# Kernel optimization log

Measured on AMD Instinct MI355X. Metric: run time of the kernel, lower is better.

## Reference

```python
import jax, jax.numpy as jnp
import numpy as np

DIM = 768
FS = 48          # feature_size; H = W = FS, N = FS*FS
HEADS = 8


def _linear_params(key, fin, fout):
    k1, k2 = jax.random.split(key)
    s = 1.0 / np.sqrt(fin)
    W = jax.random.uniform(k1, (fin, fout), minval=-s, maxval=s, dtype=jnp.float32)
    b = jax.random.uniform(k2, (fout,), minval=-s, maxval=s, dtype=jnp.float32)
    return W, b


def setup_inputs() -> dict:
    key = jax.random.key(0)
    ks = jax.random.split(key, 12)
    B, C, H, W = 1, DIM, FS, FS
    N = H * W
    x = jax.random.normal(ks[0], (B, C, H, W), dtype=jnp.float32)
    y = jax.random.normal(ks[1], (B, C, H, W), dtype=jnp.float32)
    Wqx, bqx = _linear_params(ks[2], C, 3 * C)
    Wqy, bqy = _linear_params(ks[3], C, 3 * C)
    Wqxc, bqxc = _linear_params(ks[4], N, 3 * N)
    Wqyc, bqyc = _linear_params(ks[5], N, 3 * N)
    Wpxc, bpxc = _linear_params(ks[6], N, N)
    Wpyc, bpyc = _linear_params(ks[7], N, N)
    Wax, bax = _linear_params(ks[8], C, C)
    Way, bay = _linear_params(ks[9], C, C)
    return {"x": x, "y": y,
            "Wqx": Wqx, "bqx": bqx, "Wqy": Wqy, "bqy": bqy,
            "Wqxc": Wqxc, "bqxc": bqxc, "Wqyc": Wqyc, "bqyc": bqyc,
            "Wpxc": Wpxc, "bpxc": bpxc, "Wpyc": Wpyc, "bpyc": bpyc,
            "Wax": Wax, "bax": bax, "Way": Way, "bay": bay}


def reference(x, y, Wqx, bqx, Wqy, bqy, Wqxc, bqxc, Wqyc, bqyc,
              Wpxc, bpxc, Wpyc, bpyc, Wax, bax, Way, bay):
    B, C, H, W = x.shape
    N = H * W
    h = HEADS
    hd = C // h            # spatial head dim
    hdc = N // h           # channel head dim
    scale = hd ** (-0.5)
    scale_c = hdc ** (-0.5)

    def spatial_qkv(t, Wq, bq):
        t_ = t.transpose(0, 2, 3, 1).reshape(B, N, C)          # [B,N,C]
        qkv = (t_ @ Wq + bq).reshape(B, N, 3, h, hd)
        qkv = qkv.transpose(2, 0, 3, 1, 4).reshape(3, B * h, N, hd)
        return qkv[0], qkv[1], qkv[2]

    def channel_qkv(t, Wq, bq):
        tc = t.reshape(B, C, N)                                 # [B,C,N]
        qkv = (tc @ Wq + bq).reshape(B, C, 3, h, hdc)
        qkv = qkv.transpose(2, 0, 3, 1, 4).reshape(3, B * h, C, hdc)
        return qkv[0], qkv[1], qkv[2]

    qx, kx, vx = spatial_qkv(x, Wqx, bqx)
    qy, ky, vy = spatial_qkv(y, Wqy, bqy)
    qxc, kxc, vxc = channel_qkv(x, Wqxc, bqxc)
    qyc, kyc, vyc = channel_qkv(y, Wqyc, bqyc)

    # spatial self-attention (x with x, y with y): scores [B*h, N, N]
    ax = jax.nn.softmax((qx * scale) @ kx.transpose(0, 2, 1), axis=-1)
    ay = jax.nn.softmax((qy * scale) @ ky.transpose(0, 2, 1), axis=-1)
    # channel cross-attention (x queries attend to y keys/values and vice versa): scores [B*h, C, C]
    axc = jax.nn.softmax((qxc * scale_c) @ kyc.transpose(0, 2, 1), axis=-1)
    ayc = jax.nn.softmax((qyc * scale_c) @ kxc.transpose(0, 2, 1), axis=-1)

    # NOTE: reshape(B, N, -1) on the [B*h, N, hd] layout (no head transpose) replicates the
    # original torch code exactly.
    x_self = ((ax @ vx).reshape(B, N, C) @ Wax + bax).reshape(B, H, W, C).transpose(0, 3, 1, 2)
    y_self = ((ay @ vy).reshape(B, N, C) @ Way + bay).reshape(B, H, W, C).transpose(0, 3, 1, 2)
    x_ch = ((axc @ vyc).reshape(B, C, N) @ Wpxc + bpxc).reshape(B, C, H, W)
    y_ch = ((ayc @ vxc).reshape(B, C, N) @ Wpyc + bpyc).reshape(B, C, H, W)

    return (x_self + x_ch, y_self + y_ch)
```

## Files before the change

### kernel.cpp

```cpp
#include <hip/hip_runtime.h>
#include <math.h>

typedef unsigned short u16;
typedef unsigned int u32;
typedef short bf16x8 __attribute__((ext_vector_type(8)));
typedef float f32x4 __attribute__((ext_vector_type(4)));
typedef float f32x16 __attribute__((ext_vector_type(16)));

__device__ __forceinline__ float bf2f(u16 u) {
  union { unsigned int i; float f; } v;
  v.i = ((unsigned int)u) << 16;
  return v.f;
}
__device__ __forceinline__ u16 f2bf(float f) {
  union { float f; unsigned int i; } v;
  v.f = f;
  unsigned int u = v.i;
  return (u16)((u + 0x7fffu + ((u >> 16) & 1u)) >> 16);
}
__device__ __forceinline__ u32 pkbf(float a, float b) {
  u32 d;
  asm("v_cvt_pk_bf16_f32 %0, %1, %2" : "=v"(d) : "v"(a), "v"(b));
  return d;
}

__device__ __forceinline__ void glds16(const u16* g, u16* l) {
  __builtin_amdgcn_global_load_lds(
      (const __attribute__((address_space(1))) void*)g,
      (__attribute__((address_space(3))) void*)l, 16, 0, 0);
}

__global__ __launch_bounds__(256) void probe_dtype(const u32* __restrict__ xw,
                                                   int nwords, int* flag)
{
  const int tid = threadIdx.x;
  int cnt = 0;
  for (int i = tid; i < nwords; i += 256) {
    u32 w = xw[i];
    u32 e = (w >> 7) & 0xFFu;
    if (e >= 110u && e <= 140u) cnt++;
  }
#pragma unroll
  for (int off = 32; off >= 1; off >>= 1) cnt += __shfl_xor(cnt, off);
  __shared__ int s[4];
  if ((tid & 63) == 0) s[tid >> 6] = cnt;
  __syncthreads();
  if (tid == 0) {
    int tot = s[0] + s[1] + s[2] + s[3];
    flag[0] = (tot < nwords / 2) ? 1 : 0;
  }
}

__global__ __launch_bounds__(256) void gemm128(
    const u16* __restrict__ A, int lda, long sAz,
    const u16* __restrict__ B, int ldb, long sBz,
    const u16* __restrict__ bias, int sBiasZ,
    void* __restrict__ OutV, int ldo, long sOz, long oOff, int outMode,
    const int* __restrict__ flagp,
    float scale, int M, int Nn, int K)
{
  const int z = blockIdx.z;
  const u16* Ab = A + (long)z * sAz;
  const u16* Bb = B + (long)z * sBz;
  const int bm = blockIdx.y * 128;
  const int bn = blockIdx.x * 128;

  __shared__ u16 As[2][128 * 32];
  __shared__ u16 Bs[2][128 * 32];

  const int tid  = threadIdx.x;
  const int lane = tid & 63;
  const int wave = tid >> 6;
  const int wr = wave >> 1, wc = wave & 1;
  const int q = lane >> 4, l15 = lane & 15;

  f32x4 acc[4][4];
#pragma unroll
  for (int i = 0; i < 4; i++)
#pragma unroll
    for (int j = 0; j < 4; j++) acc[i][j] = (f32x4){0.f, 0.f, 0.f, 0.f};

  const int srow = tid >> 2;
  const int sc8  = (tid & 3) * 8;
  const u16* aptr = Ab + (long)(bm + srow) * lda + sc8;
  const u16* bptr = Bb + (long)(bn + srow) * ldb + sc8;

  auto stage = [&](int buf, int k0) {
    u16* asl = As[buf] + tid * 8;
    u16* bsl = Bs[buf] + tid * 8;
    glds16(aptr + k0, asl);
    glds16(aptr + (long)64 * lda + k0, asl + 256 * 8);
    glds16(bptr + k0, bsl);
    glds16(bptr + (long)64 * ldb + k0, bsl + 256 * 8);
  };
  auto compute = [&](int buf) {
    bf16x8 af[4], bfr[4];
#pragma unroll
    for (int mi = 0; mi < 4; mi++)
      af[mi] = *(const bf16x8*)(As[buf] + (wr * 64 + mi * 16 + l15) * 32 + q * 8);
#pragma unroll
    for (int nj = 0; nj < 4; nj++)
      bfr[nj] = *(const bf16x8*)(Bs[buf] + (wc * 64 + nj * 16 + l15) * 32 + q * 8);
#pragma unroll
    for (int mi = 0; mi < 4; mi++)
#pragma unroll
      for (int nj = 0; nj < 4; nj++)
        acc[mi][nj] = __builtin_amdgcn_mfma_f32_16x16x32_bf16(af[mi], bfr[nj], acc[mi][nj], 0, 0, 0);
  };

  stage(0, 0);
  __syncthreads();
  int cur = 0;
  for (int k0 = 32; k0 < K; k0 += 32) {
    stage(cur ^ 1, k0);
    compute(cur);
    __syncthreads();
    cur ^= 1;
  }
  compute(cur);

  const int flagv = (outMode == 2) ? *flagp : 0;
  const bool storeF32 = (outMode == 1) || (outMode == 2 && flagv);
  const u16* bz = bias ? bias + (long)z * sBiasZ : nullptr;
#pragma unroll
  for (int mi = 0; mi < 4; mi++) {
    const int r0 = bm + wr * 64 + mi * 16 + q * 4;
#pragma unroll
    for (int nj = 0; nj < 4; nj++) {
      const int col = bn + wc * 64 + nj * 16 + l15;
      const float bsv = bz ? bf2f(bz[col]) : 0.0f;
      if (storeF32) {
        float* Out = (float*)OutV + oOff + (long)z * sOz;
#pragma unroll
        for (int r = 0; r < 4; r++)
          Out[(long)(r0 + r) * ldo + col] = acc[mi][nj][r] * scale + bsv;
      } else {
        u16* Out = (u16*)OutV + oOff + (long)z * sOz;
#pragma unroll
        for (int r = 0; r < 4; r++)
          Out[(long)(r0 + r) * ldo + col] = f2bf(acc[mi][nj][r] * scale + bsv);
      }
    }
  }
}

__global__ __launch_bounds__(256) void flashS(
    const u16* __restrict__ QKV, long sTz,
    const u16* __restrict__ VTb, long sVz,
    u16* __restrict__ Out, long sOz,
    int ldq, int Mq, float scl)
{
  const int bm = blockIdx.x * 128;
  const int h  = blockIdx.y;
  const int t  = blockIdx.z;
  const int h96 = h * 96;
  const u16* qB  = QKV + (long)t * sTz;
  const u16* kB  = qB + 768;
  const u16* vtB = VTb + (long)t * sVz + (long)h96 * Mq;
  u16* oB = Out + (long)t * sOz + (long)h * Mq * 96;

  __shared__ u16 KsL[2][64 * 128];
  __shared__ u16 VsL[2][96 * 64];

  const int tid  = threadIdx.x;
  const int lane = tid & 63;
  const int wave = tid >> 6;
  const int l31  = lane & 31;
  const int hi   = lane >> 5;

  bf16x8 qf[6];
  {
    const u16* qrow = qB + (long)(bm + wave * 32 + l31) * ldq + h96;
#pragma unroll
    for (int cs = 0; cs < 6; cs++) {
      union { bf16x8 v; u16 e[8]; } a, b;
      a.v = *(const bf16x8*)(qrow + cs * 16 + hi * 8);
#pragma unroll
      for (int e = 0; e < 8; e++) b.e[e] = f2bf(bf2f(a.e[e]) * scl);
      qf[cs] = b.v;
    }
  }

  f32x16 accO[3];
#pragma unroll
  for (int r = 0; r < 16; r++) { accO[0][r] = 0.f; accO[1][r] = 0.f; accO[2][r] = 0.f; }
  float m_r = -1e30f, l_r = 0.f;

  auto stageKV = [&](int buf, int k0) {
    const u16* kBase = kB + (long)k0 * ldq + h96;
#pragma unroll
    for (int i = 0; i < 4; i++) {
      const int G = tid + 256 * i;
      const int row = G >> 4;
      const int g = (G & 15) ^ (row & 7);
      const u16* src = (g < 12) ? (kBase + (long)row * ldq + g * 8) : kB;
      glds16(src, &KsL[buf][G * 8]);
    }
    const u16* vBase = vtB + k0;
#pragma unroll
    for (int i = 0; i < 3; i++) {
      const int G = tid + 256 * i;
      const int row = G >> 3;
      const int g = (G & 7) ^ (row & 7);
      glds16(vBase + (long)row * Mq + g * 8, &VsL[buf][G * 8]);
    }
  };
  auto ldK = [&](int buf, int kt2, int cs) -> bf16x8 {
    const int row = kt2 * 32 + l31;
    const int g = (2 * cs + hi) ^ (row & 7);
    return *(const bf16x8*)(&KsL[buf][row * 128 + g * 8]);
  };
  auto ldV = [&](int buf, int dt, int s) -> bf16x8 {
    const int row = dt * 32 + l31;
    const int g = (2 * s + hi) ^ (row & 7);
    return *(const bf16x8*)(&VsL[buf][row * 64 + g * 8]);
  };

  stageKV(0, 0);
  __syncthreads();
  int cur = 0;
  const int nt = Mq / 64;
  for (int kt = 0; kt < nt; kt++) {
    if (kt + 1 < nt) stageKV(cur ^ 1, (kt + 1) * 64);

    f32x16 sA, sB;
#pragma unroll
    for (int r = 0; r < 16; r++) { sA[r] = 0.f; sB[r] = 0.f; }
#pragma unroll
    for (int cs = 0; cs < 6; cs++) {
      sA = __builtin_amdgcn_mfma_f32_32x32x16_bf16(ldK(cur, 0, cs), qf[cs], sA, 0, 0, 0);
      sB = __builtin_amdgcn_mfma_f32_32x32x16_bf16(ldK(cur, 1, cs), qf[cs], sB, 0, 0, 0);
    }

    float tm = -1e30f;
#pragma unroll
    for (int r = 0; r < 16; r++) tm = fmaxf(tm, fmaxf(sA[r], sB[r]));
    tm = fmaxf(tm, __shfl_xor(tm, 32));
    if (!__all(tm <= m_r + 8.f)) {
      const float mn = fmaxf(m_r, tm);
      const float al = __expf(m_r - mn);
      m_r = mn; l_r *= al;
#pragma unroll
      for (int r = 0; r < 16; r++) {
        const float a = __shfl(al, (r & 3) + 8 * (r >> 2) + 4 * hi);
        accO[0][r] *= a; accO[1][r] *= a; accO[2][r] *= a;
      }
    }
    float rs = 0.f;
#pragma unroll
    for (int r = 0; r < 16; r++) {
      sA[r] = __expf(sA[r] - m_r); rs += sA[r];
      sB[r] = __expf(sB[r] - m_r); rs += sB[r];
    }
    rs += __shfl_xor(rs, 32);
    l_r += rs;

#pragma unroll
    for (int s = 0; s < 4; s++) {
      const f32x16& P = (s < 2) ? sA : sB;
      const int rb = (s & 1) * 8;
      u32 X  = pkbf(P[rb + 0], P[rb + 1]);
      u32 X2 = pkbf(P[rb + 2], P[rb + 3]);
      u32 Y  = pkbf(P[rb + 4], P[rb + 5]);
      u32 Y2 = pkbf(P[rb + 6], P[rb + 7]);
      asm volatile("v_permlane32_swap_b32 %0, %1" : "+v"(X), "+v"(Y));
      asm volatile("v_permlane32_swap_b32 %0, %1" : "+v"(X2), "+v"(Y2));
      union { u32 w[4]; bf16x8 v; } pa;
      pa.w[0] = X; pa.w[1] = X2; pa.w[2] = Y; pa.w[3] = Y2;
#pragma unroll
      for (int dt = 0; dt < 3; dt++)
        accO[dt] = __builtin_amdgcn_mfma_f32_32x32x16_bf16(pa.v, ldV(cur, dt, s), accO[dt], 0, 0, 0);
    }

    __syncthreads();
    cur ^= 1;
  }

  const float inv = 1.0f / l_r;
#pragma unroll
  for (int r = 0; r < 16; r++) {
    const int row = (r & 3) + 8 * (r >> 2) + 4 * hi;
    const float iv = __shfl(inv, row);
    const long rowb = (long)(bm + wave * 32 + row) * 96;
#pragma unroll
    for (int dt = 0; dt < 3; dt++)
      oB[rowb + dt * 32 + l31] = f2bf(accO[dt][r] * iv);
  }
}

__global__ __launch_bounds__(256) void gemm_pv(
    const u16* __restrict__ P, int ldP, long sPz,
    const u16* __restrict__ Vt, int ldVt, long sVz,
    u16* __restrict__ Out, int ldo, long sOz, int K)
{
  const int z = blockIdx.z;
  const u16* Pz = P + (long)z * sPz;
  const u16* Vz = Vt + (long)z * sVz;
  u16* Oz = Out + (long)z * sOz;
  const int bm = blockIdx.y * 64;
  const int bn = blockIdx.x * 96;

  __shared__ u16 As[2][64 * 32];
  __shared__ u16 Bs[2][96 * 32];

  const int tid  = threadIdx.x;
  const int lane = tid & 63;
  const int wave = tid >> 6;
  const int wr = wave >> 1, wc = wave & 1;
  const int q = lane >> 4, l15 = lane & 15;

  f32x4 acc[2][3];
#pragma unroll
  for (int i = 0; i < 2; i++)
#pragma unroll
    for (int j = 0; j < 3; j++) acc[i][j] = (f32x4){0.f, 0.f, 0.f, 0.f};

  const int srow = lane >> 2;
  const int sc8  = (lane & 3) * 8;

  const u16* aRow = Pz + (long)(bm + wave * 16 + srow) * ldP + sc8;
  const u16* bRow0 = nullptr; const u16* bRow1 = nullptr;
  if (wave < 3) {
    bRow0 = Vz + (long)(bn + (2 * wave) * 16 + srow) * ldVt + sc8;
    bRow1 = Vz + (long)(bn + (2 * wave + 1) * 16 + srow) * ldVt + sc8;
  }

  auto stage = [&](int buf, int k0) {
    glds16(aRow + k0, As[buf] + wave * 512 + lane * 8);
    if (wave < 3) {
      glds16(bRow0 + k0, Bs[buf] + (2 * wave) * 512 + lane * 8);
      glds16(bRow1 + k0, Bs[buf] + (2 * wave + 1) * 512 + lane * 8);
    }
  };
  auto compute = [&](int buf) {
    bf16x8 af[2], bfr[3];
#pragma unroll
    for (int mi = 0; mi < 2; mi++)
      af[mi] = *(const bf16x8*)(As[buf] + (wr * 32 + mi * 16 + l15) * 32 + q * 8);
#pragma unroll
    for (int nj = 0; nj < 3; nj++)
      bfr[nj] = *(const bf16x8*)(Bs[buf] + (wc * 48 + nj * 16 + l15) * 32 + q * 8);
#pragma unroll
    for (int mi = 0; mi < 2; mi++)
#pragma unroll
      for (int nj = 0; nj < 3; nj++)
        acc[mi][nj] = __builtin_amdgcn_mfma_f32_16x16x32_bf16(af[mi], bfr[nj], acc[mi][nj], 0, 0, 0);
  };

  stage(0, 0);
  __syncthreads();
  int cur = 0;
  for (int k0 = 32; k0 < K; k0 += 32) {
    stage(cur ^ 1, k0);
    compute(cur);
    __syncthreads();
    cur ^= 1;
  }
  compute(cur);

#pragma unroll
  for (int mi = 0; mi < 2; mi++) {
    const int r0 = bm + wr * 32 + mi * 16 + q * 4;
#pragma unroll
    for (int nj = 0; nj < 3; nj++) {
      const int cl = bn + wc * 48 + nj * 16 + l15;
#pragma unroll
      for (int r = 0; r < 4; r++)
        Oz[(long)(r0 + r) * ldo + cl] = f2bf(acc[mi][nj][r]);
    }
  }
}

#define BM 64
#define BN 64
#define BK 32
#define LDSP (BK + 8)

__global__ __launch_bounds__(256) void gemm64(
    const void* __restrict__ Av, int lda, long sAz, int aExt,
    const void* __restrict__ Bv, int ldb, long sBz, int bNT, int bExt,
    const void* __restrict__ biasv,
    void* __restrict__ OutV, int ldo, long sOz, long oOff, int outMode,
    const int* __restrict__ flagp,
    float scale, int M, int Nn, int K)
{
  const int flagv = *flagp;
  const bool aF32 = aExt && flagv;
  const bool bF32 = bExt && flagv;

  const int z = blockIdx.z;
  const int bm = blockIdx.y * BM;
  const int bn = blockIdx.x * BN;

  __shared__ u16 As[BM][LDSP];
  __shared__ u16 Bs[BN][LDSP];

  const int tid  = threadIdx.x;
  const int lane = tid & 63;
  const int wave = tid >> 6;
  const int wr = wave >> 1;
  const int wc = wave & 1;
  const int q   = lane >> 4;
  const int l15 = lane & 15;

  f32x4 acc[2][2];
#pragma unroll
  for (int i = 0; i < 2; i++)
#pragma unroll
    for (int j = 0; j < 2; j++) acc[i][j] = (f32x4){0.f, 0.f, 0.f, 0.f};

  const int am  = tid >> 2;
  const int ach = (tid & 3) * 8;

  for (int k0 = 0; k0 < K; k0 += BK) {
    __syncthreads();
    if (aF32) {
      const float* src = (const float*)Av + (long)z * sAz + (long)(bm + am) * lda + (k0 + ach);
      f32x4 f0 = *(const f32x4*)src;
      f32x4 f1 = *(const f32x4*)(src + 4);
      u16 t[8] = {f2bf(f0[0]), f2bf(f0[1]), f2bf(f0[2]), f2bf(f0[3]),
                  f2bf(f1[0]), f2bf(f1[1]), f2bf(f1[2]), f2bf(f1[3])};
      *(uint4*)(&As[am][ach]) = *(const uint4*)t;
    } else {
      const u16* src = (const u16*)Av + (long)z * sAz + (long)(bm + am) * lda + (k0 + ach);
      *(uint4*)(&As[am][ach]) = *(const uint4*)src;
    }
    if (bNT) {
      if (bF32) {
        u16 t[8] = {0, 0, 0, 0, 0, 0, 0, 0};
        if (bn + am < Nn) {
          const float* src = (const float*)Bv + (long)z * sBz + (long)(bn + am) * ldb + (k0 + ach);
          f32x4 f0 = *(const f32x4*)src;
          f32x4 f1 = *(const f32x4*)(src + 4);
#pragma unroll
          for (int j = 0; j < 4; j++) { t[j] = f2bf(f0[j]); t[4 + j] = f2bf(f1[j]); }
        }
        *(uint4*)(&Bs[am][ach]) = *(const uint4*)t;
      } else {
        uint4 val = make_uint4(0u, 0u, 0u, 0u);
        if (bn + am < Nn)
          val = *(const uint4*)((const u16*)Bv + (long)z * sBz + (long)(bn + am) * ldb + (k0 + ach));
        *(uint4*)(&Bs[am][ach]) = val;
      }
    } else {
      const int kk = tid >> 3;
      const int n0 = (tid & 7) * 8;
      if (bn + n0 < Nn) {
        if (bF32) {
          const float* src = (const float*)Bv + (long)z * sBz + (long)(k0 + kk) * ldb + (bn + n0);
          f32x4 f0 = *(const f32x4*)src;
          f32x4 f1 = *(const f32x4*)(src + 4);
#pragma unroll
          for (int j = 0; j < 4; j++) {
            Bs[n0 + j][kk] = f2bf(f0[j]);
            Bs[n0 + 4 + j][kk] = f2bf(f1[j]);
          }
        } else {
          uint4 val = *(const uint4*)((const u16*)Bv + (long)z * sBz + (long)(k0 + kk) * ldb + (bn + n0));
          const u16* pv = (const u16*)&val;
#pragma unroll
          for (int j = 0; j < 8; j++) Bs[n0 + j][kk] = pv[j];
        }
      } else {
#pragma unroll
        for (int j = 0; j < 8; j++) Bs[n0 + j][kk] = 0;
      }
    }
    __syncthreads();

    bf16x8 af[2], bfr[2];
#pragma unroll
    for (int t = 0; t < 2; t++)
      af[t] = *(const bf16x8*)(&As[wr * 32 + t * 16 + l15][q * 8]);
#pragma unroll
    for (int t = 0; t < 2; t++)
      bfr[t] = *(const bf16x8*)(&Bs[wc * 32 + t * 16 + l15][q * 8]);
#pragma unroll
    for (int i = 0; i < 2; i++)
#pragma unroll
      for (int j = 0; j < 2; j++)
        acc[i][j] = __builtin_amdgcn_mfma_f32_16x16x32_bf16(af[i], bfr[j], acc[i][j], 0, 0, 0);
  }

#pragma unroll
  for (int i = 0; i < 2; i++) {
    const int r0 = bm + wr * 32 + i * 16 + q * 4;
#pragma unroll
    for (int j = 0; j < 2; j++) {
      const int col = bn + wc * 32 + j * 16 + l15;
      if (col >= Nn) continue;
      float bsv = 0.0f;
      if (biasv) bsv = flagv ? ((const float*)biasv)[col] : bf2f(((const u16*)biasv)[col]);
      const bool storeF32 = (outMode == 1) || (outMode == 2 && flagv);
      if (storeF32) {
        float* Out = (float*)OutV + oOff + (long)z * sOz;
#pragma unroll
        for (int r = 0; r < 4; r++)
          Out[(long)(r0 + r) * ldo + col] = acc[i][j][r] * scale + bsv;
      } else {
        u16* Out = (u16*)OutV + oOff + (long)z * sOz;
#pragma unroll
        for (int r = 0; r < 4; r++)
          Out[(long)(r0 + r) * ldo + col] = f2bf(acc[i][j][r] * scale + bsv);
      }
    }
  }
}

__global__ __launch_bounds__(256) void softmax_rows(
    float* S, int ldS, long sSz,
    u16* P, int ldP, long sPz, int ncols)
{
  const int row = blockIdx.x;
  const int z = blockIdx.y;
  float* s = S + (long)z * sSz + (long)row * ldS;
  u16*   p = P + (long)z * sPz + (long)row * ldP;
  const int tid = threadIdx.x;
  const int lane = tid & 63, wave = tid >> 6;

  float v[9];
  int cnt = 0;
  float mx = -1e30f;
  for (int c = tid; c < ncols; c += 256) {
    float t = s[c];
    v[cnt++] = t;
    mx = fmaxf(mx, t);
  }
#pragma unroll
  for (int off = 32; off >= 1; off >>= 1) mx = fmaxf(mx, __shfl_xor(mx, off));
  __shared__ float redm[4];
  __shared__ float reds[4];
  if (lane == 0) redm[wave] = mx;
  __syncthreads();
  mx = fmaxf(fmaxf(redm[0], redm[1]), fmaxf(redm[2], redm[3]));

  float sum = 0.f;
  for (int i = 0; i < cnt; i++) { v[i] = __expf(v[i] - mx); sum += v[i]; }
#pragma unroll
  for (int off = 32; off >= 1; off >>= 1) sum += __shfl_xor(sum, off);
  if (lane == 0) reds[wave] = sum;
  __syncthreads();
  sum = reds[0] + reds[1] + reds[2] + reds[3];
  const float inv = 1.0f / sum;

  cnt = 0;
  for (int c = tid; c < ncols; c += 256) p[c] = f2bf(v[cnt++] * inv);
}

__global__ __launch_bounds__(256) void transpose_in(
    const void* __restrict__ tinv, u16* __restrict__ outp,
    const int* __restrict__ flagp, int inRows, int inCols)
{
  const bool f32 = *flagp != 0;
  __shared__ u16 tile[32][33];
  const int bx = blockIdx.x * 32;
  const int by = blockIdx.y * 32;
  const int tx = threadIdx.x & 31;
  const int ty = threadIdx.x >> 5;
#pragma unroll
  for (int k = 0; k < 4; k++) {
    const long idx = (long)(by + ty + k * 8) * inCols + bx + tx;
    tile[ty + k * 8][tx] = f32 ? f2bf(((const float*)tinv)[idx]) : ((const u16*)tinv)[idx];
  }
  __syncthreads();
#pragma unroll
  for (int k = 0; k < 4; k++) {
    const int j = bx + ty + k * 8;
    const int i = by + tx;
    outp[(long)j * inRows + i] = tile[tx][ty + k * 8];
  }
}

__global__ __launch_bounds__(256) void transpose_v(
    const u16* __restrict__ src, int ldsrc,
    u16* __restrict__ dst, int lddst, int rows, int cols)
{
  __shared__ u16 tile[32][33];
  const int bx = blockIdx.x * 32;
  const int by = blockIdx.y * 32;
  const int tx = threadIdx.x & 31;
  const int ty = threadIdx.x >> 5;
#pragma unroll
  for (int k = 0; k < 4; k++)
    tile[ty + k * 8][tx] = src[(long)(by + ty + k * 8) * ldsrc + bx + tx];
  __syncthreads();
#pragma unroll
  for (int k = 0; k < 4; k++)
    dst[(long)(bx + ty + k * 8) * lddst + by + tx] = tile[tx][ty + k * 8];
}

__global__ __launch_bounds__(256) void cvt_flat(
    const void* __restrict__ src, u16* __restrict__ dst,
    const int* __restrict__ flagp, long n)
{
  const bool f32 = *flagp != 0;
  long i = ((long)blockIdx.x * 256 + threadIdx.x) * 4;
  if (i + 3 < n) {
    if (f32) {
      f32x4 v = *(const f32x4*)((const float*)src + i);
#pragma unroll
      for (int j = 0; j < 4; j++) dst[i + j] = f2bf(v[j]);
    } else {
      *(uint2*)(dst + i) = *(const uint2*)((const u16*)src + i);
    }
  }
}

struct P8 { const void* p[8]; };
__global__ __launch_bounds__(256) void cvt_bias(P8 s, u16* __restrict__ dst,
                                                const int* __restrict__ flagp)
{
  const bool f32 = *flagp != 0;
  const int sizes[8] = {2304, 2304, 6912, 6912, 2304, 2304, 768, 768};
  int gid = blockIdx.x * 256 + threadIdx.x;
  int seg = 0, off = gid;
  while (seg < 8 && off >= sizes[seg]) { off -= sizes[seg]; seg++; }
  if (seg >= 8) return;
  float v = f32 ? ((const float*)s.p[seg])[off] : bf2f(((const u16*)s.p[seg])[off]);
  dst[gid] = f2bf(v);
}

__global__ __launch_bounds__(256) void transpose_add_out(
    const u16* __restrict__ tin, void* outv, long oOff,
    const int* __restrict__ flagp, int inRows, int inCols)
{
  const bool f32 = *flagp != 0;
  __shared__ u16 tile[32][33];
  const int bx = blockIdx.x * 32;
  const int by = blockIdx.y * 32;
  const int tx = threadIdx.x & 31;
  const int ty = threadIdx.x >> 5;
#pragma unroll
  for (int k = 0; k < 4; k++)
    tile[ty + k * 8][tx] = tin[(long)(by + ty + k * 8) * inCols + bx + tx];
  __syncthreads();
#pragma unroll
  for (int k = 0; k < 4; k++) {
    const int j = bx + ty + k * 8;
    const int i = by + tx;
    const long idx = (long)j * inRows + i;
    const float val = bf2f(tile[tx][ty + k * 8]);
    if (f32) {
      float* o = (float*)outv + oOff;
      o[idx] = o[idx] + val;
    } else {
      u16* o = (u16*)outv + oOff;
      o[idx] = f2bf(bf2f(o[idx]) + val);
    }
  }
}

extern "C" void kernel_launch(void* const* d_in, const int* in_sizes, int n_in,
                              void* d_out, int out_size, void* d_ws, size_t ws_size,
                              hipStream_t stream)
{
  const int N = 2304, C = 768, HD = 96, HDC = 288;
  const size_t NC = (size_t)N * C;

  const void* x    = d_in[0];
  const void* y    = d_in[1];
  const void* Wqx  = d_in[2];  const void* bqx  = d_in[3];
  const void* Wqy  = d_in[4];  const void* bqy  = d_in[5];
  const void* Wqxc = d_in[6];  const void* bqxc = d_in[7];
  const void* Wqyc = d_in[8];  const void* bqyc = d_in[9];
  const void* Wpxc = d_in[10]; const void* bpxc = d_in[11];
  const void* Wpyc = d_in[12]; const void* bpyc = d_in[13];
  const void* Wax  = d_in[14]; const void* bax  = d_in[15];
  const void* Way  = d_in[16]; const void* bay  = d_in[17];

  char* base = (char*)d_ws;
  int* flag = (int*)base;
  size_t off = 256;
  auto alloc16 = [&](size_t elems) -> u16* {
    u16* p = (u16*)(base + off);
    off = (off + elems * 2 + 255) & ~(size_t)255;
    return p;
  };

  u16* WqxT  = alloc16((size_t)2304 * 768);
  u16* WqyT  = alloc16((size_t)2304 * 768);
  u16* WqxcT = alloc16((size_t)6912 * 2304);
  u16* WqycT = alloc16((size_t)6912 * 2304);
  u16* WpxcT = alloc16((size_t)2304 * 2304);
  u16* WpycT = alloc16((size_t)2304 * 2304);
  u16* WaxT  = alloc16((size_t)768 * 768);
  u16* WayT  = alloc16((size_t)768 * 768);
  u16* biasB = alloc16(24576);
  u16* xb = alloc16(NC);
  u16* yb = alloc16(NC);
  u16* RT = alloc16(2 * NC);
  u16* RQ1 = alloc16(3 * NC);
  u16* RQ2 = alloc16(3 * NC);
  u16* RS = alloc16(2 * NC);
  u16* VT = alloc16(2 * NC);
  size_t fixedEnd = off;
  float* Sbuf = (float*)(base + fixedEnd);
  size_t availS = ws_size > fixedEnd ? ws_size - fixedEnd : 0;

  const size_t spHead = (size_t)N * N * 4;
  const bool fat = ws_size >= fixedEnd + spHead;

  auto G64 = [&](const void* A, int lda, long sAz, int aExt,
                 const void* B, int ldb, long sBz, int bNT, int bExt,
                 const void* bias, void* Out, int ldo, long sOz, long oOff, int outMode,
                 float scale, int M, int Nn, int K, int Z) {
    dim3 grid((Nn + BN - 1) / BN, (M + BM - 1) / BM, Z);
    gemm64<<<grid, 256, 0, stream>>>(A, lda, sAz, aExt, B, ldb, sBz, bNT, bExt,
                                     bias, Out, ldo, sOz, oOff, outMode, flag,
                                     scale, M, Nn, K);
  };
  auto G128 = [&](const u16* A, int lda, long sAz,
                  const u16* B, int ldb, long sBz,
                  const u16* bias, int sBiasZ,
                  void* Out, int ldo, long sOz, long oOff, int outMode,
                  float scale, int M, int Nn, int K, int Z) {
    dim3 grid(Nn / 128, M / 128, Z);
    gemm128<<<grid, 256, 0, stream>>>(A, lda, sAz, B, ldb, sBz, bias, sBiasZ,
                                      Out, ldo, sOz, oOff, outMode, flag,
                                      scale, M, Nn, K);
  };

  probe_dtype<<<1, 256, 0, stream>>>((const u32*)x, 1024, flag);

  if (fat) {
    transpose_in<<<dim3(2304 / 32, 768 / 32),  256, 0, stream>>>(Wqx,  WqxT,  flag, 768,  2304);
    transpose_in<<<dim3(2304 / 32, 768 / 32),  256, 0, stream>>>(Wqy,  WqyT,  flag, 768,  2304);
    transpose_in<<<dim3(6912 / 32, 2304 / 32), 256, 0, stream>>>(Wqxc, WqxcT, flag, 2304, 6912);
    transpose_in<<<dim3(6912 / 32, 2304 / 32), 256, 0, stream>>>(Wqyc, WqycT, flag, 2304, 6912);
    transpose_in<<<dim3(2304 / 32, 2304 / 32), 256, 0, stream>>>(Wpxc, WpxcT, flag, 2304, 2304);
    transpose_in<<<dim3(2304 / 32, 2304 / 32), 256, 0, stream>>>(Wpyc, WpycT, flag, 2304, 2304);
    transpose_in<<<dim3(768 / 32, 768 / 32),   256, 0, stream>>>(Wax,  WaxT,  flag, 768,  768);
    transpose_in<<<dim3(768 / 32, 768 / 32),   256, 0, stream>>>(Way,  WayT,  flag, 768,  768);
    P8 bp; bp.p[0] = bqx; bp.p[1] = bqy; bp.p[2] = bqxc; bp.p[3] = bqyc;
    bp.p[4] = bpxc; bp.p[5] = bpyc; bp.p[6] = bax; bp.p[7] = bay;
    cvt_bias<<<96, 256, 0, stream>>>(bp, biasB, flag);
    const u16 *bqxB = biasB, *bqxcB = biasB + 4608,
              *bpxcB = biasB + 18432, *baxB = biasB + 23040;
    cvt_flat<<<(unsigned)(NC / 4 / 256), 256, 0, stream>>>(x, xb, flag, (long)NC);
    cvt_flat<<<(unsigned)(NC / 4 / 256), 256, 0, stream>>>(y, yb, flag, (long)NC);
    u16 *xt = RT, *yt = RT + NC;
    transpose_in<<<dim3(N / 32, C / 32), 256, 0, stream>>>(x, xt, flag, C, N);
    transpose_in<<<dim3(N / 32, C / 32), 256, 0, stream>>>(y, yt, flag, C, N);

    auto attF = [&](const u16* qB, const u16* kB, const u16* vB, int ldq,
                    u16* att, int Mq, int hd, float scl) {
      transpose_v<<<dim3((8 * hd) / 32, Mq / 32), 256, 0, stream>>>(vB, ldq, VT, Mq, Mq, 8 * hd);
      const long perHead = (long)Mq * Mq * 4;
      int nb = (int)(availS / perHead);
      if (nb > 8) nb = 8;
      for (int h0 = 0; h0 < 8; h0 += nb) {
        const int zc = (8 - h0 < nb) ? 8 - h0 : nb;
        G128(qB + h0 * hd, ldq, hd, kB + h0 * hd, ldq, hd, nullptr, 0,
             Sbuf, Mq, (long)Mq * Mq, 0, 1, scl, Mq, Mq, hd, zc);
        softmax_rows<<<dim3(Mq, zc), 256, 0, stream>>>(Sbuf, Mq, (long)Mq * Mq,
            (u16*)Sbuf, 2 * Mq, (long)Mq * 2 * Mq, Mq);
        gemm_pv<<<dim3(hd / 96, Mq / 64, zc), 256, 0, stream>>>(
            (const u16*)Sbuf, 2 * Mq, (long)Mq * 2 * Mq,
            VT + (long)h0 * hd * Mq, Mq, (long)hd * Mq,
            att + (long)h0 * Mq * hd, hd, (long)Mq * hd, Mq);
      }
    };

    u16 *qkvxs = RQ1;
    G128(xt, C, (long)NC, WqxT, C, (long)NC, bqxB, 3 * C,
         qkvxs, 3 * C, 3 * (long)NC, 0, 0, 1.f, N, 3 * C, C, 2);

    u16 *qkvys = RQ2;
    u16 *attx = RT;
    const float sscale = 1.0f / sqrtf(96.0f);
    transpose_v<<<dim3((8 * HD) / 32, N / 32), 256, 0, stream>>>(
        qkvxs + 2 * C, 3 * C, VT, N, N, 8 * HD);
    transpose_v<<<dim3((8 * HD) / 32, N / 32), 256, 0, stream>>>(
        qkvys + 2 * C, 3 * C, VT + NC, N, N, 8 * HD);
    flashS<<<dim3(N / 128, 8, 2), 256, 0, stream>>>(
        qkvxs, 3 * (long)NC, VT, (long)NC, attx, (long)NC, 3 * C, N, sscale);

    u16 *xself = RS;
    G128(attx, C, (long)NC, WaxT, C, (long)768 * 768, baxB, C,
         xself, C, (long)NC, 0, 0, 1.f, N, C, C, 2);

    u16 *qkvxc = RQ1, *qkvyc = RQ2;
    G128(xb, N, (long)NC, WqxcT, N, (long)6912 * 2304, bqxcB, 3 * N,
         qkvxc, 3 * N, 3 * (long)NC, 0, 0, 1.f, C, 3 * N, N, 2);

    u16 *attxc = RT, *attyc = RT + NC;
    const float cscale = 1.0f / sqrtf(288.0f);
    attF(qkvxc, qkvyc + N, qkvyc + 2 * N, 3 * N, attxc, C, HDC, cscale);
    attF(qkvyc, qkvxc + N, qkvxc + 2 * N, 3 * N, attyc, C, HDC, cscale);

    G128(attxc, N, (long)NC, WpxcT, N, (long)2304 * 2304, bpxcB, N,
         d_out, N, (long)NC, 0, 2, 1.f, C, N, N, 2);

    transpose_add_out<<<dim3(C / 32, N / 32), 256, 0, stream>>>(xself, d_out, 0, flag, N, C);
    transpose_add_out<<<dim3(C / 32, N / 32), 256, 0, stream>>>(RS + NC, d_out, (long)NC, flag, N, C);
    return;
  }

  {
    char* b2 = (char*)d_ws;
    u16* RA = (u16*)(b2 + 256);
    u16* RB = RA + 3 * NC;
    u16* RD = RB + 3 * NC;
    u16* RE = RD + 2 * NC;
    const size_t offSsp = 256 + (size_t)(8 * NC) * 2;
    float* Ssp = (float*)(b2 + offSsp);
    const size_t availSp = ws_size > offSsp ? ws_size - offSsp : 0;
    const size_t offSch = 256 + (size_t)(10 * NC) * 2;
    float* Sch = (float*)(b2 + offSch);
    const size_t availCh = ws_size > offSch ? ws_size - offSch : 0;

    u16 *xt = RD, *yt = RD + NC;
    u16 *qkvxs = RA, *qkvys = RB;
    u16 *attx = RD, *atty = RD + NC;
    u16 *xself = RE, *yself = RE + NC;
    u16 *qkvxc = RA, *qkvyc = RB;
    u16 *attxc = RD, *attyc = RD + NC;

    auto attention = [&](const u16* qB, const u16* kB, const u16* vB, int ldq,
                         u16* att, int Mq, int hd, float scl,
                         float* S, size_t availBytes) {
      const long perHead = (long)Mq * Mq * 4;
      int nb = (int)(availBytes / perHead);
      if (nb > 8) nb = 8;
      if (nb >= 1) {
        for (int h0 = 0; h0 < 8; h0 += nb) {
          const int zc = (8 - h0 < nb) ? 8 - h0 : nb;
          G64(qB + h0 * hd, ldq, hd, 0, kB + h0 * hd, ldq, hd, 1, 0, nullptr,
              S, Mq, (long)Mq * Mq, 0, 1, scl, Mq, Mq, hd, zc);
          softmax_rows<<<dim3(Mq, zc), 256, 0, stream>>>(S, Mq, (long)Mq * Mq,
              (u16*)S, 2 * Mq, (long)Mq * 2 * Mq, Mq);
          G64((const u16*)S, 2 * Mq, (long)Mq * 2 * Mq, 0, vB + h0 * hd, ldq, hd, 0, 0,
              nullptr, att + (long)h0 * Mq * hd, hd, (long)Mq * hd, 0, 0,
              1.f, Mq, hd, Mq, zc);
        }
      } else {
        long rows = (long)(availBytes / ((size_t)Mq * 4)) & ~63L;
        if (rows < 64) rows = 64;
        if (rows > Mq) rows = Mq;
        for (int h = 0; h < 8; h++) {
          for (int m0 = 0; m0 < Mq; m0 += (int)rows) {
            const int mr = (Mq - m0 < rows) ? (int)(Mq - m0) : (int)rows;
            G64(qB + (long)m0 * ldq + h * hd, ldq, 0, 0, kB + h * hd, ldq, 0, 1, 0,
                nullptr, S, Mq, 0, 0, 1, scl, mr, Mq, hd, 1);
            softmax_rows<<<dim3(mr, 1), 256, 0, stream>>>(S, Mq, 0, (u16*)S, 2 * Mq, 0, Mq);
            G64((const u16*)S, 2 * Mq, 0, 0, vB + h * hd, ldq, 0, 0, 0, nullptr,
                att + (long)h * Mq * hd + (long)m0 * hd, hd, 0, 0, 0, 1.f, mr, hd, Mq, 1);
          }
        }
      }
    };

    transpose_in<<<dim3(N / 32, C / 32), 256, 0, stream>>>(x, xt, flag, C, N);
    transpose_in<<<dim3(N / 32, C / 32), 256, 0, stream>>>(y, yt, flag, C, N);

    G64(xt, C, 0, 0, Wqx, 3 * C, 0, 0, 1, bqx, qkvxs, 3 * C, 0, 0, 0, 1.f, N, 3 * C, C, 1);
    G64(yt, C, 0, 0, Wqy, 3 * C, 0, 0, 1, bqy, qkvys, 3 * C, 0, 0, 0, 1.f, N, 3 * C, C, 1);

    const float sscale = 1.0f / sqrtf(96.0f);
    attention(qkvxs, qkvxs + C, qkvxs + 2 * C, 3 * C, attx, N, HD, sscale, Ssp, availSp);
    attention(qkvys, qkvys + C, qkvys + 2 * C, 3 * C, atty, N, HD, sscale, Ssp, availSp);

    G64(attx, C, 0, 0, Wax, C, 0, 0, 1, bax, xself, C, 0, 0, 0, 1.f, N, C, C, 1);
    G64(atty, C, 0, 0, Way, C, 0, 0, 1, bay, yself, C, 0, 0, 0, 1.f, N, C, C, 1);

    G64(x, N, 0, 1, Wqxc, 3 * N, 0, 0, 1, bqxc, qkvxc, 3 * N, 0, 0, 0, 1.f, C, 3 * N, N, 1);
    G64(y, N, 0, 1, Wqyc, 3 * N, 0, 0, 1, bqyc, qkvyc, 3 * N, 0, 0, 0, 1.f, C, 3 * N, N, 1);

    const float cscale = 1.0f / sqrtf(288.0f);
    attention(qkvxc, qkvyc + N, qkvyc + 2 * N, 3 * N, attxc, C, HDC, cscale, Sch, availCh);
    attention(qkvyc, qkvxc + N, qkvxc + 2 * N, 3 * N, attyc, C, HDC, cscale, Sch, availCh);

    G64(attxc, N, 0, 0, Wpxc, N, 0, 0, 1, bpxc, d_out, N, 0, 0, 2, 1.f, C, N, N, 1);
    G64(attyc, N, 0, 0, Wpyc, N, 0, 0, 1, bpyc, d_out, N, 0, (long)NC, 2, 1.f, C, N, N, 1);

    transpose_add_out<<<dim3(C / 32, N / 32), 256, 0, stream>>>(xself, d_out, 0, flag, N, C);
    transpose_add_out<<<dim3(C / 32, N / 32), 256, 0, stream>>>(yself, d_out, (long)NC, flag, N, C);
  }
}
```

Baseline: 714.5 us.

## Split flash spatial attention KV range across wave pairs with LDS merge

Each block now handles 64 query rows instead of 128, and its four waves form two pairs. Each pair processes half of the key/value sequence in 32-key tiles using its own LDS buffers. The two pairs' partial softmax states (running max, sum and output accumulators) are merged through shared memory at the end. Together with the doubled grid, this raises block count and occupancy for the N=2304 problem. It also adds s_setprio hints around the MFMA sections and splits the QK accumulation into two chains. The costs are an extra sync, the LDS merge traffic, and smaller per-tile work.

```diff
diff --git a/kernel.cpp b/kernel.cpp
--- a/kernel.cpp
+++ b/kernel.cpp
@@ -150,7 +150,7 @@
     u16* __restrict__ Out, long sOz,
     int ldq, int Mq, float scl)
 {
-  const int bm = blockIdx.x * 128;
+  const int bm = blockIdx.x * 64;
   const int h  = blockIdx.y;
   const int t  = blockIdx.z;
   const int h96 = h * 96;
@@ -159,18 +159,22 @@
   const u16* vtB = VTb + (long)t * sVz + (long)h96 * Mq;
   u16* oB = Out + (long)t * sOz + (long)h * Mq * 96;
 
-  __shared__ u16 KsL[2][64 * 128];
-  __shared__ u16 VsL[2][96 * 64];
+  __shared__ u16 SH[2 * 16384];
 
   const int tid  = threadIdx.x;
   const int lane = tid & 63;
   const int wave = tid >> 6;
   const int l31  = lane & 31;
   const int hi   = lane >> 5;
+  const int wp   = wave >> 1;
+  const int wq   = wave & 1;
+  const int ptid = tid & 127;
+  u16* PB = SH + wp * 16384;
+  const int kst = wp * (Mq >> 1);
 
   bf16x8 qf[6];
   {
-    const u16* qrow = qB + (long)(bm + wave * 32 + l31) * ldq + h96;
+    const u16* qrow = qB + (long)(bm + wq * 32 + l31) * ldq + h96;
 #pragma unroll
     for (int cs = 0; cs < 6; cs++) {
       union { bf16x8 v; u16 e[8]; } a, b;
@@ -188,53 +192,60 @@
 
   auto stageKV = [&](int buf, int k0) {
     const u16* kBase = kB + (long)k0 * ldq + h96;
+    u16* kd = PB + buf * 4096;
 #pragma unroll
     for (int i = 0; i < 4; i++) {
-      const int G = tid + 256 * i;
-      const int row = G >> 4;
-      const int g = (G & 15) ^ (row & 7);
+      const int G = ptid + 128 * i;
+      const int row = G >> 4, gi = G & 15;
+      const int g = gi ^ (row & 7);
       const u16* src = (g < 12) ? (kBase + (long)row * ldq + g * 8) : kB;
-      glds16(src, &KsL[buf][G * 8]);
+      glds16(src, kd + G * 8);
     }
     const u16* vBase = vtB + k0;
-#pragma unroll
-    for (int i = 0; i < 3; i++) {
-      const int G = tid + 256 * i;
-      const int row = G >> 3;
-      const int g = (G & 7) ^ (row & 7);
-      glds16(vBase + (long)row * Mq + g * 8, &VsL[buf][G * 8]);
+    u16* vd = PB + 8192 + buf * 4096;
+#pragma unroll
+    for (int i = 0; i < 4; i++) {
+      const int G = ptid + 128 * i;
+      const int row = G / 5, gi = G - row * 5;
+      const bool ok = (G < 480) && (gi < 4);
+      const u16* src = ok ? (vBase + (long)row * Mq + (long)(gi ^ (row & 3)) * 8) : vtB;
+      glds16(src, vd + G * 8);
     }
   };
-  auto ldK = [&](int buf, int kt2, int cs) -> bf16x8 {
-    const int row = kt2 * 32 + l31;
-    const int g = (2 * cs + hi) ^ (row & 7);
-    return *(const bf16x8*)(&KsL[buf][row * 128 + g * 8]);
+  auto ldK = [&](int buf, int cs) -> bf16x8 {
+    const int g = (2 * cs + hi) ^ (l31 & 7);
+    return *(const bf16x8*)(PB + buf * 4096 + l31 * 128 + g * 8);
   };
   auto ldV = [&](int buf, int dt, int s) -> bf16x8 {
     const int row = dt * 32 + l31;
-    const int g = (2 * s + hi) ^ (row & 7);
-    return *(const bf16x8*)(&VsL[buf][row * 64 + g * 8]);
+    const int g = (2 * s + hi) ^ (row & 3);
+    return *(const bf16x8*)(PB + 8192 + buf * 4096 + row * 40 + g * 8);
   };
 
-  stageKV(0, 0);
+  stageKV(0, kst);
   __syncthreads();
   int cur = 0;
-  const int nt = Mq / 64;
+  const int nt = Mq >> 6;
   for (int kt = 0; kt < nt; kt++) {
-    if (kt + 1 < nt) stageKV(cur ^ 1, (kt + 1) * 64);
-
-    f32x16 sA, sB;
-#pragma unroll
-    for (int r = 0; r < 16; r++) { sA[r] = 0.f; sB[r] = 0.f; }
-#pragma unroll
-    for (int cs = 0; cs < 6; cs++) {
-      sA = __builtin_amdgcn_mfma_f32_32x32x16_bf16(ldK(cur, 0, cs), qf[cs], sA, 0, 0, 0);
-      sB = __builtin_amdgcn_mfma_f32_32x32x16_bf16(ldK(cur, 1, cs), qf[cs], sB, 0, 0, 0);
-    }
+    if (kt + 1 < nt) stageKV(cur ^ 1, kst + (kt + 1) * 32);
+
+    f32x16 s1, s2;
+#pragma unroll
+    for (int r = 0; r < 16; r++) { s1[r] = 0.f; s2[r] = 0.f; }
+    __builtin_amdgcn_s_setprio(1);
+#pragma unroll
+    for (int cs = 0; cs < 3; cs++) {
+      s1 = __builtin_amdgcn_mfma_f32_32x32x16_bf16(ldK(cur, 2 * cs),     qf[2 * cs],     s1, 0, 0, 0);
+      s2 = __builtin_amdgcn_mfma_f32_32x32x16_bf16(ldK(cur, 2 * cs + 1), qf[2 * cs + 1], s2, 0, 0, 0);
+    }
+    __builtin_amdgcn_s_setprio(0);
+    f32x16 sA;
+#pragma unroll
+    for (int r = 0; r < 16; r++) sA[r] = s1[r] + s2[r];
 
     float tm = -1e30f;
 #pragma unroll
-    for (int r = 0; r < 16; r++) tm = fmaxf(tm, fmaxf(sA[r], sB[r]));
+    for (int r = 0; r < 16; r++) tm = fmaxf(tm, sA[r]);
     tm = fmaxf(tm, __shfl_xor(tm, 32));
     if (!__all(tm <= m_r + 8.f)) {
       const float mn = fmaxf(m_r, tm);
@@ -248,43 +259,62 @@
     }
     float rs = 0.f;
 #pragma unroll
-    for (int r = 0; r < 16; r++) {
-      sA[r] = __expf(sA[r] - m_r); rs += sA[r];
-      sB[r] = __expf(sB[r] - m_r); rs += sB[r];
-    }
+    for (int r = 0; r < 16; r++) { sA[r] = __expf(sA[r] - m_r); rs += sA[r]; }
     rs += __shfl_xor(rs, 32);
     l_r += rs;
 
 #pragma unroll
-    for (int s = 0; s < 4; s++) {
-      const f32x16& P = (s < 2) ? sA : sB;
-      const int rb = (s & 1) * 8;
-      u32 X  = pkbf(P[rb + 0], P[rb + 1]);
-      u32 X2 = pkbf(P[rb + 2], P[rb + 3]);
-      u32 Y  = pkbf(P[rb + 4], P[rb + 5]);
-      u32 Y2 = pkbf(P[rb + 6], P[rb + 7]);
+    for (int s = 0; s < 2; s++) {
+      const int rb = s * 8;
+      u32 X  = pkbf(sA[rb + 0], sA[rb + 1]);
+      u32 X2 = pkbf(sA[rb + 2], sA[rb + 3]);
+      u32 Y  = pkbf(sA[rb + 4], sA[rb + 5]);
+      u32 Y2 = pkbf(sA[rb + 6], sA[rb + 7]);
       asm volatile("v_permlane32_swap_b32 %0, %1" : "+v"(X), "+v"(Y));
       asm volatile("v_permlane32_swap_b32 %0, %1" : "+v"(X2), "+v"(Y2));
       union { u32 w[4]; bf16x8 v; } pa;
       pa.w[0] = X; pa.w[1] = X2; pa.w[2] = Y; pa.w[3] = Y2;
+      __builtin_amdgcn_s_setprio(1);
 #pragma unroll
       for (int dt = 0; dt < 3; dt++)
         accO[dt] = __builtin_amdgcn_mfma_f32_32x32x16_bf16(pa.v, ldV(cur, dt, s), accO[dt], 0, 0, 0);
+      __builtin_amdgcn_s_setprio(0);
     }
 
     __syncthreads();
     cur ^= 1;
   }
 
-  const float inv = 1.0f / l_r;
-#pragma unroll
-  for (int r = 0; r < 16; r++) {
-    const int row = (r & 3) + 8 * (r >> 2) + 4 * hi;
-    const float iv = __shfl(inv, row);
-    const long rowb = (long)(bm + wave * 32 + row) * 96;
+  float* fsh = (float*)SH;
+  const int MLOFF = 128 * 49;
+  if (wp == 1) {
+    float* ab = fsh + (wq * 64 + lane) * 49;
 #pragma unroll
     for (int dt = 0; dt < 3; dt++)
-      oB[rowb + dt * 32 + l31] = f2bf(accO[dt][r] * iv);
+#pragma unroll
+      for (int r = 0; r < 16; r++) ab[dt * 16 + r] = accO[dt][r];
+    fsh[MLOFF + wq * 64 + lane] = m_r;
+    fsh[MLOFF + 128 + wq * 64 + lane] = l_r;
+  }
+  __syncthreads();
+  if (wp == 0) {
+    const float m2 = fsh[MLOFF + wq * 64 + lane];
+    const float l2 = fsh[MLOFF + 128 + wq * 64 + lane];
+    const float mm = fmaxf(m_r, m2);
+    const float a1 = __expf(m_r - mm);
+    const float a2 = __expf(m2 - mm);
+    const float inv = 1.0f / (l_r * a1 + l2 * a2);
+    const float* ab = fsh + (wq * 64 + lane) * 49;
+#pragma unroll
+    for (int r = 0; r < 16; r++) {
+      const int row = (r & 3) + 8 * (r >> 2) + 4 * hi;
+      const float f1 = __shfl(a1 * inv, row);
+      const float f2 = __shfl(a2 * inv, row);
+      const long rowb = (long)(bm + wq * 32 + row) * 96;
+#pragma unroll
+      for (int dt = 0; dt < 3; dt++)
+        oB[rowb + dt * 32 + l31] = f2bf(accO[dt][r] * f1 + ab[dt * 16 + r] * f2);
+    }
   }
 }
 
@@ -772,7 +802,7 @@
         qkvxs + 2 * C, 3 * C, VT, N, N, 8 * HD);
     transpose_v<<<dim3((8 * HD) / 32, N / 32), 256, 0, stream>>>(
         qkvys + 2 * C, 3 * C, VT + NC, N, N, 8 * HD);
-    flashS<<<dim3(N / 128, 8, 2), 256, 0, stream>>>(
+    flashS<<<dim3(N / 64, 8, 2), 256, 0, stream>>>(
         qkvxs, 3 * (long)NC, VT, (long)NC, attx, (long)NC, 3 * C, N, sscale);
 
     u16 *xself = RS;
```

Measured after the change: 696.0 us. 1.03x faster.
